# Performance work log

Measured on AMD Instinct MI355X. Metric: run time of the kernel, lower is better.

## Reference

```python
import jax, jax.numpy as jnp
import numpy as np

TANH_SCALAR = 10.0  # taug in IrEne eq. 1 (close_to_one setting)

N_NODES = 2**21 - 1   # complete binary tree, depth D=21
N_LEAVES = 2**20
NUM_FEATURES = 64


def setup_inputs() -> dict:
    key = jax.random.key(0)
    k1, k2, k3, k4 = jax.random.split(key, 4)
    features = jax.random.normal(k1, (N_NODES, NUM_FEATURES), dtype=jnp.float32)
    leaf_energy = jax.random.uniform(k2, (N_LEAVES,), dtype=jnp.float32)
    W = jax.random.normal(k3, (NUM_FEATURES, 1), dtype=jnp.float32) * 0.1
    b = jax.random.normal(k4, (1,), dtype=jnp.float32) * 0.1
    return {"features": features, "leaf_energy": leaf_energy, "W": W, "b": b}


def reference(features, leaf_energy, W, b):
    """Batched equivalent of RecursiveTreeComputation (close_to_one, end2end).

    Tree layout: complete binary tree in level order; node i's parent is (i-1)//2.
    Level d occupies indices [2^d - 1, 2^{d+1} - 1). Leaves are the last level.
    parent_energy = sum_children score(child) * child_energy,
    score(f) = 1 + tanh(f @ W + b) / tanh_scalar.
    Returns predicted energy for every node, shape [N].
    """
    N, F = features.shape
    D = int(np.log2(N + 1))  # number of levels (static)

    # One fused pass over all nodes: Linear(F,1) + tanh + affine (WeightingModel).
    scores = 1.0 + jnp.tanh(features @ W + b)[:, 0] / TANH_SCALAR  # [N]

    leaf_start = 2 ** (D - 1) - 1
    energy = jnp.zeros((N,), dtype=features.dtype).at[leaf_start:].set(leaf_energy)

    # Level-wise bottom-up accumulation; consecutive child pairs share a parent.
    for d in range(D - 1, 0, -1):
        start, end = 2 ** d - 1, 2 ** (d + 1) - 1          # children at level d
        contrib = scores[start:end] * energy[start:end]      # weighted child energies
        parent_vals = contrib.reshape(-1, 2).sum(axis=1)     # sum sibling pairs
        pstart = 2 ** (d - 1) - 1                             # parents at level d-1
        energy = energy.at[pstart:start].set(energy[pstart:start] + parent_vals)
    return energy
```

## Files before the change

kernel.cpp:

```cpp
#include <hip/hip_runtime.h>
#include <cmath>

#define N_NODES_C   ((1 << 21) - 1)
#define N_LEAVES_C  (1 << 20)
#define LEAF_START  (N_LEAVES_C - 1)
#define NFEAT       64

__device__ __forceinline__ float score_fn(float dot, float bias) {
    return 1.0f + tanhf(dot + bias) * 0.1f;
}

__global__ __launch_bounds__(256) void score_stream_kernel(
        const float* __restrict__ features,
        const float* __restrict__ leaf_energy,
        const float* __restrict__ W,
        const float* __restrict__ b,
        float* __restrict__ ws,
        float* __restrict__ out) {
    const int q = threadIdx.x & 7;
    const float4 wl = ((const float4*)W)[q];
    const float4 wh = ((const float4*)W)[q + 8];
    const float bias = b[0];
    const int g0 = (blockIdx.x * 256 + threadIdx.x) >> 3;
    const int gstride = (gridDim.x * 256) >> 3;
    for (int node = g0; node < N_NODES_C; node += gstride) {
        const float4* fp = (const float4*)(features + (size_t)node * NFEAT);
        const float4 a = fp[q];
        const float4 c = fp[q + 8];
        float v = a.x * wl.x + a.y * wl.y + a.z * wl.z + a.w * wl.w
                + c.x * wh.x + c.y * wh.y + c.z * wh.z + c.w * wh.w;
        v += __shfl_xor(v, 1);
        v += __shfl_xor(v, 2);
        v += __shfl_xor(v, 4);
        if (q == 0) {
            const float s = score_fn(v, bias);
            if (node >= LEAF_START) {
                const float e = leaf_energy[node - LEAF_START];
                ws[node] = s * e;
                out[node] = e;
            } else {
                ws[node] = s;
            }
        }
    }
}

__global__ __launch_bounds__(256) void mid_reduce_kernel(
        const float* __restrict__ ws,
        float* __restrict__ out) {
    __shared__ float sc[1024];
    __shared__ float buf[2][1024];
    const int tid = threadIdx.x;
    const int blk = blockIdx.x;

    const int lbase = LEAF_START + (blk << 10);
    for (int i = tid; i < 1024; i += 256)
        buf[0][i] = ws[lbase + i];

    for (int pd = 19; pd >= 11; --pd) {
        const int m = 1 << (pd - 10);
        const int gbase = ((1 << pd) - 1) + blk * m;
        const int off = 1024 - 2 * m;
        for (int j = tid; j < m; j += 256)
            sc[off + j] = ws[gbase + j];
    }

    int p = 0;
    for (int pd = 19; pd >= 10; --pd) {
        const int m = 1 << (pd - 10);
        __syncthreads();
        const int gbase = ((1 << pd) - 1) + blk * m;
        for (int j = tid; j < m; j += 256) {
            const float val = buf[p][2 * j] + buf[p][2 * j + 1];
            out[gbase + j] = val;
            if (pd > 10)
                buf[1 - p][j] = sc[(1024 - 2 * m) + j] * val;
        }
        p ^= 1;
    }
}

__global__ __launch_bounds__(1024) void top_reduce_kernel(
        const float* __restrict__ ws,
        float* __restrict__ out) {
    __shared__ float sc[2048];
    __shared__ float buf[2][1024];
    const int tid = threadIdx.x;
    for (int i = tid; i < 2047; i += 1024)
        sc[i] = ws[i];
    buf[0][tid] = out[1023 + tid];
    __syncthreads();
    buf[0][tid] = sc[1023 + tid] * buf[0][tid];

    int p = 0;
    for (int pd = 9; pd >= 0; --pd) {
        const int m = 1 << pd;
        __syncthreads();
        const int base = m - 1;
        for (int j = tid; j < m; j += 1024) {
            const float val = buf[p][2 * j] + buf[p][2 * j + 1];
            out[base + j] = val;
            if (pd > 0)
                buf[1 - p][j] = sc[base + j] * val;
        }
        p ^= 1;
    }
}

extern "C" void kernel_launch(void* const* d_in, const int* in_sizes, int n_in,
                              void* d_out, int out_size, void* d_ws, size_t ws_size,
                              hipStream_t stream) {
    (void)in_sizes; (void)n_in; (void)out_size; (void)ws_size;
    const float* features    = (const float*)d_in[0];
    const float* leaf_energy = (const float*)d_in[1];
    const float* W           = (const float*)d_in[2];
    const float* b           = (const float*)d_in[3];
    float* out = (float*)d_out;
    float* ws  = (float*)d_ws;

    score_stream_kernel<<<8192, 256, 0, stream>>>(features, leaf_energy, W, b, ws, out);
    mid_reduce_kernel<<<1024, 256, 0, stream>>>(ws, out);
    top_reduce_kernel<<<1, 1024, 0, stream>>>(ws, out);
}
```

Measured before the change: 701.1 us.

## Use nontemporal feature loads, move leaf handling to reduce kernel, rebalance tree split

Feature rows are now read with nontemporal loads because they are streamed once. The leaf-energy read and output write move out of the score kernel into the mid-level reduction, so the streaming kernel only writes scores. The mid reduction now handles 512-leaf subtrees across 2048 blocks, and the single-block top kernel takes one more level, 11 instead of 10. This trades more parallelism in the mid stage for a longer serial top stage.

```diff
diff --git a/kernel.cpp b/kernel.cpp
--- a/kernel.cpp
+++ b/kernel.cpp
@@ -6,75 +6,71 @@
 #define LEAF_START  (N_LEAVES_C - 1)
 #define NFEAT       64
 
+typedef float f32x4 __attribute__((ext_vector_type(4)));
+
 __device__ __forceinline__ float score_fn(float dot, float bias) {
     return 1.0f + tanhf(dot + bias) * 0.1f;
 }
 
 __global__ __launch_bounds__(256) void score_stream_kernel(
         const float* __restrict__ features,
-        const float* __restrict__ leaf_energy,
         const float* __restrict__ W,
         const float* __restrict__ b,
-        float* __restrict__ ws,
-        float* __restrict__ out) {
+        float* __restrict__ ws) {
     const int q = threadIdx.x & 7;
-    const float4 wl = ((const float4*)W)[q];
-    const float4 wh = ((const float4*)W)[q + 8];
+    const f32x4 wl = ((const f32x4*)W)[q];
+    const f32x4 wh = ((const f32x4*)W)[q + 8];
     const float bias = b[0];
     const int g0 = (blockIdx.x * 256 + threadIdx.x) >> 3;
     const int gstride = (gridDim.x * 256) >> 3;
     for (int node = g0; node < N_NODES_C; node += gstride) {
-        const float4* fp = (const float4*)(features + (size_t)node * NFEAT);
-        const float4 a = fp[q];
-        const float4 c = fp[q + 8];
+        const f32x4* fp = (const f32x4*)(features + (size_t)node * NFEAT);
+        const f32x4 a = __builtin_nontemporal_load(fp + q);
+        const f32x4 c = __builtin_nontemporal_load(fp + q + 8);
         float v = a.x * wl.x + a.y * wl.y + a.z * wl.z + a.w * wl.w
                 + c.x * wh.x + c.y * wh.y + c.z * wh.z + c.w * wh.w;
         v += __shfl_xor(v, 1);
         v += __shfl_xor(v, 2);
         v += __shfl_xor(v, 4);
-        if (q == 0) {
-            const float s = score_fn(v, bias);
-            if (node >= LEAF_START) {
-                const float e = leaf_energy[node - LEAF_START];
-                ws[node] = s * e;
-                out[node] = e;
-            } else {
-                ws[node] = s;
-            }
-        }
+        if (q == 0) ws[node] = score_fn(v, bias);
     }
 }
 
 __global__ __launch_bounds__(256) void mid_reduce_kernel(
         const float* __restrict__ ws,
+        const float* __restrict__ leaf_energy,
         float* __restrict__ out) {
-    __shared__ float sc[1024];
-    __shared__ float buf[2][1024];
+    __shared__ float sc[512];
+    __shared__ float buf[2][512];
     const int tid = threadIdx.x;
     const int blk = blockIdx.x;
 
-    const int lbase = LEAF_START + (blk << 10);
-    for (int i = tid; i < 1024; i += 256)
-        buf[0][i] = ws[lbase + i];
+    const int l0 = blk << 9;
+    for (int i = tid; i < 512; i += 256) {
+        const float e = leaf_energy[l0 + i];
+        const float s = ws[LEAF_START + l0 + i];
+        out[LEAF_START + l0 + i] = e;
+        buf[0][i] = s * e;
+    }
 
-    for (int pd = 19; pd >= 11; --pd) {
-        const int m = 1 << (pd - 10);
+    for (int pd = 19; pd >= 12; --pd) {
+        const int m = 1 << (pd - 11);
         const int gbase = ((1 << pd) - 1) + blk * m;
-        const int off = 1024 - 2 * m;
+        const int off = 512 - 2 * m;
         for (int j = tid; j < m; j += 256)
             sc[off + j] = ws[gbase + j];
     }
 
     int p = 0;
-    for (int pd = 19; pd >= 10; --pd) {
-        const int m = 1 << (pd - 10);
+    for (int pd = 19; pd >= 11; --pd) {
+        const int m = 1 << (pd - 11);
         __syncthreads();
         const int gbase = ((1 << pd) - 1) + blk * m;
         for (int j = tid; j < m; j += 256) {
             const float val = buf[p][2 * j] + buf[p][2 * j + 1];
             out[gbase + j] = val;
-            if (pd > 10)
-                buf[1 - p][j] = sc[(1024 - 2 * m) + j] * val;
+            if (pd > 11)
+                buf[1 - p][j] = sc[(512 - 2 * m) + j] * val;
         }
         p ^= 1;
     }
@@ -83,17 +79,19 @@
 __global__ __launch_bounds__(1024) void top_reduce_kernel(
         const float* __restrict__ ws,
         float* __restrict__ out) {
-    __shared__ float sc[2048];
-    __shared__ float buf[2][1024];
+    __shared__ float sc[4095];
+    __shared__ float buf[2][2048];
     const int tid = threadIdx.x;
-    for (int i = tid; i < 2047; i += 1024)
+    const float e0 = out[2047 + tid];
+    const float e1 = out[3071 + tid];
+    for (int i = tid; i < 4095; i += 1024)
         sc[i] = ws[i];
-    buf[0][tid] = out[1023 + tid];
     __syncthreads();
-    buf[0][tid] = sc[1023 + tid] * buf[0][tid];
+    buf[0][tid]        = sc[2047 + tid] * e0;
+    buf[0][tid + 1024] = sc[3071 + tid] * e1;
 
     int p = 0;
-    for (int pd = 9; pd >= 0; --pd) {
+    for (int pd = 10; pd >= 0; --pd) {
         const int m = 1 << pd;
         __syncthreads();
         const int base = m - 1;
@@ -118,7 +116,7 @@
     float* out = (float*)d_out;
     float* ws  = (float*)d_ws;
 
-    score_stream_kernel<<<8192, 256, 0, stream>>>(features, leaf_energy, W, b, ws, out);
-    mid_reduce_kernel<<<1024, 256, 0, stream>>>(ws, out);
+    score_stream_kernel<<<8192, 256, 0, stream>>>(features, W, b, ws);
+    mid_reduce_kernel<<<2048, 256, 0, stream>>>(ws, leaf_energy, out);
     top_reduce_kernel<<<1, 1024, 0, stream>>>(ws, out);
 }
```

New measurement: 666.6 us. 4.9% less time.
